# Kernel optimization log

Hardware: AMD Instinct MI355X
Metric: run time of the kernel (lower is better)

The kernel has to match this reference:

```python
import jax, jax.numpy as jnp
import numpy as np

C = 1024
H = 16
HS = C // H
HID = 4096
A_MIX = 0.7
B_MIX = 0.3
EPS = 1e-5


def layernorm(x, w, b):
    mu = jnp.mean(x, axis=-1, keepdims=True)
    var = jnp.mean(jnp.square(x - mu), axis=-1, keepdims=True)
    return (x - mu) * jax.lax.rsqrt(var + EPS) * w + b


def setup_inputs() -> dict:
    key = jax.random.key(0)
    ks = jax.random.split(key, 12)
    B, N = 4, 1024
    s = 1.0 / np.sqrt(C)
    sh = 1.0 / np.sqrt(HID)
    return {
        "x": jax.random.normal(ks[0], (B, N, C), jnp.float32),
        "Query": jax.random.normal(ks[1], (B, H, N, HS), jnp.float32),
        "Key": jax.random.normal(ks[2], (B, H, N, HS), jnp.float32),
        "Value": jax.random.normal(ks[3], (B, H, N, HS), jnp.float32),
        "ln_w": jnp.ones((C,), jnp.float32),
        "ln_b": jnp.zeros((C,), jnp.float32),
        "qk_w": jax.random.normal(ks[4], (2 * C, C), jnp.float32) * s,
        "qk_b": jnp.zeros((2 * C,), jnp.float32),
        "v_w": jax.random.normal(ks[5], (C, C), jnp.float32) * s,
        "v_b": jnp.zeros((C,), jnp.float32),
        "out_w": jax.random.normal(ks[6], (C, C), jnp.float32) * s,
        "out_b": jnp.zeros((C,), jnp.float32),
        "mlp_w1": jax.random.normal(ks[7], (HID, C), jnp.float32) * s,
        "mlp_b1": jnp.zeros((HID,), jnp.float32),
        "mlp_w2": jax.random.normal(ks[8], (C, HID), jnp.float32) * sh,
        "mlp_b2": jnp.zeros((C,), jnp.float32),
    }


def reference(x, Query, Key, Value, ln_w, ln_b, qk_w, qk_b, v_w, v_b,
              out_w, out_b, mlp_w1, mlp_b1, mlp_w2, mlp_b2):
    B, N, _ = x.shape
    x1 = x
    xn = layernorm(x, ln_w, ln_b)
    # qk projection -> view (B,N,H,HS,2), permute -> (2,B,H,N,HS)
    qk = (xn @ qk_w.T + qk_b).reshape(B, N, H, HS, 2)
    Q = jnp.transpose(qk[..., 0], (0, 2, 1, 3))  # (B,H,N,HS)
    K = jnp.transpose(qk[..., 1], (0, 2, 1, 3))
    V = jnp.transpose((xn @ v_w.T + v_b).reshape(B, N, H, HS), (0, 2, 1, 3))
    Query = A_MIX * Q + B_MIX * Query
    Key = A_MIX * K + B_MIX * Key
    Value = B_MIX * Value + A_MIX * V
    attn = jnp.einsum('bhqd,bhkd->bhqk', Query, Key) / np.sqrt(HS)
    attn = jax.nn.softmax(attn, axis=-1)  # dropout = identity in eval
    o = jnp.einsum('bhqk,bhkd->bhqd', attn, Value)
    o = jnp.transpose(o, (0, 2, 1, 3)).reshape(B, N, C)
    o = o @ out_w.T + out_b
    x = x1 + o
    x2 = x
    xn2 = layernorm(x, ln_w, ln_b)  # same layernorm params reused
    h = jax.nn.gelu(xn2 @ mlp_w1.T + mlp_b1, approximate=False)
    m = h @ mlp_w2.T + mlp_b2
    return (m + x2, Query, Key, Value)
```

## Files before the change

kernel.cpp:

```cpp
#include <hip/hip_runtime.h>

using bf16x8 = __attribute__((ext_vector_type(8))) __bf16;
using f32x4  = __attribute__((ext_vector_type(4))) float;

#define AS1(p) (const __attribute__((address_space(1))) void*)(p)
#define AS3(p) (__attribute__((address_space(3))) void*)(p)

__device__ __forceinline__ unsigned short f2bf(float f) {
    unsigned int u = __float_as_uint(f);
    unsigned int r = (u + 0x7FFFu + ((u >> 16) & 1u)) >> 16;
    return (unsigned short)r;
}
__device__ __forceinline__ float bf2f(unsigned short u) {
    return __uint_as_float((unsigned int)u << 16);
}

__global__ __launch_bounds__(256) void cvt_kernel(const float* __restrict__ in,
                                                  unsigned short* __restrict__ out,
                                                  int n) {
    int i = (blockIdx.x * 256 + threadIdx.x) * 4;
    if (i < n) {
        float4 v = *(const float4*)(in + i);
        ushort4 o = make_ushort4(f2bf(v.x), f2bf(v.y), f2bf(v.z), f2bf(v.w));
        *(ushort4*)(out + i) = o;
    }
}

__global__ __launch_bounds__(256) void ln_kernel(const float* __restrict__ in,
                                                 const float* __restrict__ w,
                                                 const float* __restrict__ b,
                                                 unsigned short* __restrict__ out) {
    const int row = blockIdx.x;
    const int tid = threadIdx.x;
    const float4 v = *(const float4*)(in + (size_t)row * 1024 + tid * 4);
    float s  = v.x + v.y + v.z + v.w;
    float ss = v.x * v.x + v.y * v.y + v.z * v.z + v.w * v.w;
    #pragma unroll
    for (int m = 1; m < 64; m <<= 1) {
        s  += __shfl_xor(s, m, 64);
        ss += __shfl_xor(ss, m, 64);
    }
    __shared__ float red[8];
    if ((tid & 63) == 0) { red[(tid >> 6) * 2] = s; red[(tid >> 6) * 2 + 1] = ss; }
    __syncthreads();
    s  = red[0] + red[2] + red[4] + red[6];
    ss = red[1] + red[3] + red[5] + red[7];
    const float mu  = s * (1.0f / 1024.0f);
    const float var = ss * (1.0f / 1024.0f) - mu * mu;
    const float rstd = rsqrtf(var + 1e-5f);
    const float4 wv = *(const float4*)(w + tid * 4);
    const float4 bv = *(const float4*)(b + tid * 4);
    ushort4 o;
    o.x = f2bf((v.x - mu) * rstd * wv.x + bv.x);
    o.y = f2bf((v.y - mu) * rstd * wv.y + bv.y);
    o.z = f2bf((v.z - mu) * rstd * wv.z + bv.z);
    o.w = f2bf((v.w - mu) * rstd * wv.w + bv.w);
    *(ushort4*)(out + (size_t)row * 1024 + tid * 4) = o;
}

template <int EPI>
__global__ __launch_bounds__(256, 4)
void gemm_bt(const unsigned short* __restrict__ A,
             const unsigned short* __restrict__ W,
             const float* __restrict__ bias,
             int M, int N, int K,
             const float* __restrict__ e0, const float* __restrict__ e1,
             float* __restrict__ o0, float* __restrict__ o1,
             unsigned short* __restrict__ u0, unsigned short* __restrict__ u1) {
    __shared__ unsigned short As0[128 * 32];
    __shared__ unsigned short Bs0[128 * 32];
    __shared__ unsigned short As1[128 * 32];
    __shared__ unsigned short Bs1[128 * 32];
    const int tid  = threadIdx.x;
    const int wave = tid >> 6, lane = tid & 63;
    const int wr = wave >> 1, wc = wave & 1;
    const int q15 = lane & 15, g = lane >> 4;
    const int gm0 = blockIdx.y * 128, gn0 = blockIdx.x * 128;

    f32x4 acc[4][4] = {};

    const int srow16 = lane >> 2;
    const int sslot  = (((lane & 3) ^ (srow16 & 3) ^ ((srow16 >> 2) & 3)) << 3);
    const int rx     = ((q15 ^ (q15 >> 2)) & 3) << 4;

    const unsigned short* Arow = A + (size_t)(gm0 + wave * 32 + srow16) * K + sslot;
    const unsigned short* Wrow = W + (size_t)(gn0 + wave * 32 + srow16) * K + sslot;
    const size_t rstep = (size_t)16 * K;

    #define STAGE(kt, Asb, Bsb)                                                         \
        {                                                                               \
            const int k0_ = (kt) * 32;                                                  \
            __builtin_amdgcn_global_load_lds(AS1(Arow + k0_),                           \
                AS3((char*)Asb + wave * 2048), 16, 0, 0);                               \
            __builtin_amdgcn_global_load_lds(AS1(Arow + rstep + k0_),                   \
                AS3((char*)Asb + wave * 2048 + 1024), 16, 0, 0);                        \
            __builtin_amdgcn_global_load_lds(AS1(Wrow + k0_),                           \
                AS3((char*)Bsb + wave * 2048), 16, 0, 0);                               \
            __builtin_amdgcn_global_load_lds(AS1(Wrow + rstep + k0_),                   \
                AS3((char*)Bsb + wave * 2048 + 1024), 16, 0, 0);                        \
        }

    #define COMPUTE(Asb, Bsb)                                                           \
        {                                                                               \
            bf16x8 af[4], bfr[4];                                                       \
            _Pragma("unroll")                                                           \
            for (int m = 0; m < 4; ++m)                                                 \
                af[m] = *(const bf16x8*)((char*)Asb +                                   \
                         (wr * 64 + m * 16 + q15) * 64 + ((g << 4) ^ rx));              \
            _Pragma("unroll")                                                           \
            for (int n = 0; n < 4; ++n)                                                 \
                bfr[n] = *(const bf16x8*)((char*)Bsb +                                  \
                         (wc * 64 + n * 16 + q15) * 64 + ((g << 4) ^ rx));              \
            _Pragma("unroll")                                                           \
            for (int m = 0; m < 4; ++m)                                                 \
                _Pragma("unroll")                                                       \
                for (int n = 0; n < 4; ++n)                                             \
                    acc[m][n] = __builtin_amdgcn_mfma_f32_16x16x32_bf16(                \
                        af[m], bfr[n], acc[m][n], 0, 0, 0);                             \
        }

    const int nt = K >> 5;
    STAGE(0, As0, Bs0);
    __syncthreads();
    for (int t = 0; t + 2 < nt; t += 2) {
        STAGE(t + 1, As1, Bs1);
        COMPUTE(As0, Bs0);
        __syncthreads();
        STAGE(t + 2, As0, Bs0);
        COMPUTE(As1, Bs1);
        __syncthreads();
    }
    STAGE(nt - 1, As1, Bs1);
    COMPUTE(As0, Bs0);
    __syncthreads();
    COMPUTE(As1, Bs1);
    #undef STAGE
    #undef COMPUTE

    #pragma unroll
    for (int m = 0; m < 4; ++m)
    #pragma unroll
    for (int n = 0; n < 4; ++n)
    #pragma unroll
    for (int j = 0; j < 4; ++j) {
        const int r = gm0 + wr * 64 + m * 16 + g * 4 + j;
        const int c = gn0 + wc * 64 + n * 16 + q15;
        const float val = acc[m][n][j] + bias[c];
        if constexpr (EPI == 0) {
            const int bb = r >> 10, nn = r & 1023;
            const int h = c >> 7, hs = (c >> 1) & 63, isk = c & 1;
            const size_t idx = (((size_t)(bb * 16 + h)) * 1024 + nn) * 64 + hs;
            if (!isk) { const float mx = 0.7f * val + 0.3f * e0[idx]; o0[idx] = mx; u0[idx] = f2bf(mx); }
            else      { const float mx = 0.7f * val + 0.3f * e1[idx]; o1[idx] = mx; u1[idx] = f2bf(mx); }
        } else if constexpr (EPI == 1) {
            const int bb = r >> 10, nn = r & 1023;
            const int h = c >> 6, hs = c & 63;
            const size_t idx = (((size_t)(bb * 16 + h)) * 1024 + nn) * 64 + hs;
            const float mx = 0.7f * val + 0.3f * e0[idx];
            o0[idx] = mx;
            u0[(((size_t)(bb * 16 + h)) * 64 + hs) * 1024 + nn] = f2bf(mx);
        } else if constexpr (EPI == 2) {
            const size_t idx = (size_t)r * N + c;
            o0[idx] = val + e0[idx];
        } else if constexpr (EPI == 3) {
            const float gg = 0.5f * val * (1.0f + erff(val * 0.70710678118f));
            u0[(size_t)r * N + c] = f2bf(gg);
        } else {
            const size_t idx = (size_t)r * N + c;
            o0[idx] = val + e0[idx];
        }
    }
}

__global__ __launch_bounds__(256, 6)
void attn_kernel(const unsigned short* __restrict__ Qb,
                 const unsigned short* __restrict__ Kb,
                 const unsigned short* __restrict__ Vt,
                 unsigned short* __restrict__ Op,
                 float* __restrict__ Mws,
                 float* __restrict__ Lws) {
    const int bh = blockIdx.y;
    const int z  = blockIdx.z;
    const int tid = threadIdx.x, wave = tid >> 6, lane = tid & 63;
    const int qbase = blockIdx.x * 64 + wave * 16;
    const int q15 = lane & 15, g = lane >> 4;

    const unsigned short* Qh = Qb + (size_t)bh * 1024 * 64;
    const unsigned short* Kh = Kb + (size_t)bh * 1024 * 64;
    const unsigned short* Vh = Vt + (size_t)bh * 64 * 1024;

    __shared__ alignas(128) unsigned short Ks[64 * 64];
    __shared__ alignas(128) unsigned short Vs[64 * 64];
    __shared__ alignas(128) unsigned short Ps[4][1024];
    char* const Pb = (char*)Ps[wave] + q15 * 128;
    const int swz = (q15 & 7) << 4;

    const int srow8 = lane >> 3;
    const int selm  = (((lane & 7) ^ srow8) << 3);

    bf16x8 aq[2];
    aq[0] = *(const bf16x8*)&Qh[(size_t)(qbase + q15) * 64 + 0  + g * 8];
    aq[1] = *(const bf16x8*)&Qh[(size_t)(qbase + q15) * 64 + 32 + g * 8];

    f32x4 o[4] = {};
    float mrow = -1e30f, lrow = 0.f;

    const int t0 = z * 8;
    for (int t = t0; t < t0 + 8; ++t) {
        const int kb = t * 64;
        #pragma unroll
        for (int i = 0; i < 2; ++i) {
            const int r = wave * 16 + i * 8 + srow8;
            __builtin_amdgcn_global_load_lds(AS1(Kh + (size_t)(kb + r) * 64 + selm),
                                             AS3((char*)Ks + wave * 2048 + i * 1024), 16, 0, 0);
            __builtin_amdgcn_global_load_lds(AS1(Vh + (size_t)r * 1024 + kb + selm),
                                             AS3((char*)Vs + wave * 2048 + i * 1024), 16, 0, 0);
        }
        __syncthreads();

        f32x4 s[4] = {};
        #pragma unroll
        for (int kt = 0; kt < 4; ++kt) {
            #pragma unroll
            for (int kk = 0; kk < 2; ++kk) {
                const bf16x8 bk = *(const bf16x8*)((char*)Ks + (kt * 16 + q15) * 128 +
                                                   ((kk * 64 + g * 16) ^ swz));
                s[kt] = __builtin_amdgcn_mfma_f32_16x16x32_bf16(bk, aq[kk], s[kt], 0, 0, 0);
            }
        }
        float pm = -1e30f;
        #pragma unroll
        for (int kt = 0; kt < 4; ++kt) {
            s[kt] *= 0.125f;
            pm = fmaxf(pm, fmaxf(fmaxf(s[kt][0], s[kt][1]), fmaxf(s[kt][2], s[kt][3])));
        }
        pm = fmaxf(pm, __shfl_xor(pm, 16, 64));
        pm = fmaxf(pm, __shfl_xor(pm, 32, 64));
        const float mnew = fmaxf(mrow, pm);
        const float alpha = __expf(mrow - mnew);
        mrow = mnew;

        float rs = 0.f;
        #pragma unroll
        for (int kt = 0; kt < 4; ++kt) {
            const float p0 = __expf(s[kt][0] - mnew);
            const float p1 = __expf(s[kt][1] - mnew);
            const float p2 = __expf(s[kt][2] - mnew);
            const float p3 = __expf(s[kt][3] - mnew);
            rs += (p0 + p1) + (p2 + p3);
            uint2 pk;
            pk.x = (unsigned int)f2bf(p0) | ((unsigned int)f2bf(p1) << 16);
            pk.y = (unsigned int)f2bf(p2) | ((unsigned int)f2bf(p3) << 16);
            *(uint2*)(Pb + (((kt * 32 + g * 8) ^ swz))) = pk;
        }
        rs += __shfl_xor(rs, 16, 64);
        rs += __shfl_xor(rs, 32, 64);
        lrow = lrow * alpha + rs;

        float af[4];
        #pragma unroll
        for (int j = 0; j < 4; ++j) af[j] = __shfl(alpha, g * 4 + j, 64);
        #pragma unroll
        for (int dt = 0; dt < 4; ++dt)
            #pragma unroll
            for (int j = 0; j < 4; ++j) o[dt][j] *= af[j];

        #pragma unroll
        for (int Bb = 0; Bb < 2; ++Bb) {
            const bf16x8 pa = *(const bf16x8*)(Pb + (((Bb * 64 + g * 16) ^ swz)));
            #pragma unroll
            for (int dt = 0; dt < 4; ++dt) {
                const bf16x8 vb = *(const bf16x8*)((char*)Vs + (dt * 16 + q15) * 128 +
                                                   ((Bb * 64 + g * 16) ^ swz));
                o[dt] = __builtin_amdgcn_mfma_f32_16x16x32_bf16(pa, vb, o[dt], 0, 0, 0);
            }
        }
        __syncthreads();
    }

    #pragma unroll
    for (int dt = 0; dt < 4; ++dt)
        #pragma unroll
        for (int j = 0; j < 4; ++j) {
            const int q = qbase + g * 4 + j;
            Op[(((size_t)z * 64 + bh) * 1024 + q) * 64 + dt * 16 + q15] = f2bf(o[dt][j]);
        }
    if (g == 0) {
        const size_t mi = ((size_t)z * 64 + bh) * 1024 + qbase + q15;
        Mws[mi] = mrow;
        Lws[mi] = lrow;
    }
}

__global__ __launch_bounds__(256)
void attn_combine(const unsigned short* __restrict__ Op,
                  const float* __restrict__ Mws,
                  const float* __restrict__ Lws,
                  unsigned short* __restrict__ Ob) {
    const int e4 = blockIdx.x * 256 + threadIdx.x;
    const int d0 = (e4 & 15) * 4;
    const int q  = (e4 >> 4) & 1023;
    const int bh = e4 >> 14;
    const size_t base0 = (((size_t)bh) * 1024 + q) * 64 + d0;
    const size_t base1 = (((size_t)(64 + bh)) * 1024 + q) * 64 + d0;
    const ushort4 a = *(const ushort4*)&Op[base0];
    const ushort4 c = *(const ushort4*)&Op[base1];
    const size_t mi0 = (size_t)bh * 1024 + q;
    const size_t mi1 = mi0 + 64 * 1024;
    const float m0 = Mws[mi0], m1 = Mws[mi1];
    const float l0 = Lws[mi0], l1 = Lws[mi1];
    const float m  = fmaxf(m0, m1);
    const float w0 = __expf(m0 - m), w1 = __expf(m1 - m);
    const float inv = 1.0f / (l0 * w0 + l1 * w1);
    ushort4 r;
    r.x = f2bf((bf2f(a.x) * w0 + bf2f(c.x) * w1) * inv);
    r.y = f2bf((bf2f(a.y) * w0 + bf2f(c.y) * w1) * inv);
    r.z = f2bf((bf2f(a.z) * w0 + bf2f(c.z) * w1) * inv);
    r.w = f2bf((bf2f(a.w) * w0 + bf2f(c.w) * w1) * inv);
    const int b = bh >> 4, h = bh & 15;
    *(ushort4*)&Ob[((size_t)(b * 1024 + q)) * 1024 + h * 64 + d0] = r;
}

extern "C" void kernel_launch(void* const* d_in, const int* in_sizes, int n_in,
                              void* d_out, int out_size, void* d_ws, size_t ws_size,
                              hipStream_t stream) {
    (void)in_sizes; (void)n_in; (void)out_size; (void)ws_size;
    const float* x     = (const float*)d_in[0];
    const float* Qin   = (const float*)d_in[1];
    const float* Kin   = (const float*)d_in[2];
    const float* Vin   = (const float*)d_in[3];
    const float* ln_w  = (const float*)d_in[4];
    const float* ln_b  = (const float*)d_in[5];
    const float* qk_w  = (const float*)d_in[6];
    const float* qk_b  = (const float*)d_in[7];
    const float* v_w   = (const float*)d_in[8];
    const float* v_b   = (const float*)d_in[9];
    const float* out_w = (const float*)d_in[10];
    const float* out_b = (const float*)d_in[11];
    const float* w1    = (const float*)d_in[12];
    const float* b1    = (const float*)d_in[13];
    const float* w2    = (const float*)d_in[14];
    const float* b2    = (const float*)d_in[15];

    const size_t FOUR_M = (size_t)4 * 1024 * 1024;
    float* out0 = (float*)d_out;
    float* Qout = out0 + FOUR_M;
    float* Kout = Qout + FOUR_M;
    float* Vout = Kout + FOUR_M;

    char* ws = (char*)d_ws;
    const size_t MB = 1024 * 1024;
    unsigned short* xn   = (unsigned short*)(ws + 0);
    unsigned short* qkwb = (unsigned short*)(ws + 8 * MB);
    unsigned short* vwb  = (unsigned short*)(ws + 12 * MB);
    unsigned short* owb  = (unsigned short*)(ws + 14 * MB);
    unsigned short* w1b  = (unsigned short*)(ws + 16 * MB);
    unsigned short* w2b  = (unsigned short*)(ws + 24 * MB);
    unsigned short* Qbuf = (unsigned short*)(ws + 32 * MB);
    unsigned short* Kbuf = (unsigned short*)(ws + 40 * MB);
    unsigned short* Vtb  = (unsigned short*)(ws + 48 * MB);
    unsigned short* atto = (unsigned short*)(ws + 56 * MB);
    unsigned short* hbuf = (unsigned short*)(ws + 32 * MB);
    float* y1 = (float*)(ws + 64 * MB);
    unsigned short* Oprt = (unsigned short*)(ws + 64 * MB);
    float* Mws = (float*)(ws + 8 * MB);
    float* Lws = (float*)(ws + 8 * MB + 512 * 1024);

    cvt_kernel<<<2048, 256, 0, stream>>>(qk_w, qkwb, 2048 * 1024);
    cvt_kernel<<<1024, 256, 0, stream>>>(v_w,  vwb,  1024 * 1024);
    cvt_kernel<<<1024, 256, 0, stream>>>(out_w, owb, 1024 * 1024);
    cvt_kernel<<<4096, 256, 0, stream>>>(w1, w1b, 4096 * 1024);
    cvt_kernel<<<4096, 256, 0, stream>>>(w2, w2b, 4096 * 1024);

    ln_kernel<<<4096, 256, 0, stream>>>(x, ln_w, ln_b, xn);

    {
        dim3 g(2048 / 128, 4096 / 128);
        gemm_bt<0><<<g, 256, 0, stream>>>(xn, qkwb, qk_b, 4096, 2048, 1024,
                                          Qin, Kin, Qout, Kout, Qbuf, Kbuf);
    }
    {
        dim3 g(1024 / 128, 4096 / 128);
        gemm_bt<1><<<g, 256, 0, stream>>>(xn, vwb, v_b, 4096, 1024, 1024,
                                          Vin, nullptr, Vout, nullptr, Vtb, nullptr);
    }
    {
        dim3 g(16, 64, 2);
        attn_kernel<<<g, 256, 0, stream>>>(Qbuf, Kbuf, Vtb, Oprt, Mws, Lws);
        attn_combine<<<4096, 256, 0, stream>>>(Oprt, Mws, Lws, atto);
    }
    {
        dim3 g(1024 / 128, 4096 / 128);
        gemm_bt<2><<<g, 256, 0, stream>>>(atto, owb, out_b, 4096, 1024, 1024,
                                          x, nullptr, y1, nullptr, nullptr, nullptr);
    }
    ln_kernel<<<4096, 256, 0, stream>>>(y1, ln_w, ln_b, xn);
    {
        dim3 g(4096 / 128, 4096 / 128);
        gemm_bt<3><<<g, 256, 0, stream>>>(xn, w1b, b1, 4096, 4096, 1024,
                                          nullptr, nullptr, nullptr, nullptr, hbuf, nullptr);
    }
    {
        dim3 g(1024 / 128, 4096 / 128);
        gemm_bt<4><<<g, 256, 0, stream>>>(hbuf, w2b, b2, 4096, 1024, 4096,
                                          y1, nullptr, out0, nullptr, nullptr, nullptr);
    }
}
```

Measured before the change: 308.6 us.

## Deepen GEMM LDS pipeline to four stages with explicit vmcnt waits

Replaces the double-buffered LDS staging in the bf16 GEMM with a four-deep ring buffer. Explicit s_waitcnt vmcnt counts and raw s_barrier calls replace __syncthreads, so up to three tiles of global-to-LDS loads stay in flight while one is computed. The LDS swizzle pattern is also changed, and launch bounds drop from 4 to 2 blocks per SM to fit the doubled shared memory. This trades occupancy for deeper latency hiding. The hand-written waitcnt logic assumes exactly four loads per stage and that the compiler emits no other vector memory ops in the loop.

```diff
diff --git a/kernel.cpp b/kernel.cpp
--- a/kernel.cpp
+++ b/kernel.cpp
@@ -59,7 +59,7 @@
 }
 
 template <int EPI>
-__global__ __launch_bounds__(256, 4)
+__global__ __launch_bounds__(256, 2)
 void gemm_bt(const unsigned short* __restrict__ A,
              const unsigned short* __restrict__ W,
              const float* __restrict__ bias,
@@ -67,10 +67,8 @@
              const float* __restrict__ e0, const float* __restrict__ e1,
              float* __restrict__ o0, float* __restrict__ o1,
              unsigned short* __restrict__ u0, unsigned short* __restrict__ u1) {
-    __shared__ unsigned short As0[128 * 32];
-    __shared__ unsigned short Bs0[128 * 32];
-    __shared__ unsigned short As1[128 * 32];
-    __shared__ unsigned short Bs1[128 * 32];
+    __shared__ unsigned short As[4][128 * 32];
+    __shared__ unsigned short Bs[4][128 * 32];
     const int tid  = threadIdx.x;
     const int wave = tid >> 6, lane = tid & 63;
     const int wr = wave >> 1, wc = wave & 1;
@@ -79,37 +77,36 @@
 
     f32x4 acc[4][4] = {};
 
-    const int srow16 = lane >> 2;
-    const int sslot  = (((lane & 3) ^ (srow16 & 3) ^ ((srow16 >> 2) & 3)) << 3);
-    const int rx     = ((q15 ^ (q15 >> 2)) & 3) << 4;
-
-    const unsigned short* Arow = A + (size_t)(gm0 + wave * 32 + srow16) * K + sslot;
-    const unsigned short* Wrow = W + (size_t)(gn0 + wave * 32 + srow16) * K + sslot;
+    const int selm = (((lane & 3) ^ ((lane >> 3) & 3)) << 3);
+    const int rx   = ((q15 >> 1) & 3) << 4;
+
+    const unsigned short* Arow = A + (size_t)(gm0 + wave * 32 + (lane >> 2)) * K + selm;
+    const unsigned short* Wrow = W + (size_t)(gn0 + wave * 32 + (lane >> 2)) * K + selm;
     const size_t rstep = (size_t)16 * K;
 
-    #define STAGE(kt, Asb, Bsb)                                                         \
+    #define STAGE(kt, b)                                                                \
         {                                                                               \
             const int k0_ = (kt) * 32;                                                  \
             __builtin_amdgcn_global_load_lds(AS1(Arow + k0_),                           \
-                AS3((char*)Asb + wave * 2048), 16, 0, 0);                               \
+                AS3((char*)As[b] + wave * 2048), 16, 0, 0);                             \
             __builtin_amdgcn_global_load_lds(AS1(Arow + rstep + k0_),                   \
-                AS3((char*)Asb + wave * 2048 + 1024), 16, 0, 0);                        \
+                AS3((char*)As[b] + wave * 2048 + 1024), 16, 0, 0);                      \
             __builtin_amdgcn_global_load_lds(AS1(Wrow + k0_),                           \
-                AS3((char*)Bsb + wave * 2048), 16, 0, 0);                               \
+                AS3((char*)Bs[b] + wave * 2048), 16, 0, 0);                             \
             __builtin_amdgcn_global_load_lds(AS1(Wrow + rstep + k0_),                   \
-                AS3((char*)Bsb + wave * 2048 + 1024), 16, 0, 0);                        \
-        }
-
-    #define COMPUTE(Asb, Bsb)                                                           \
+                AS3((char*)Bs[b] + wave * 2048 + 1024), 16, 0, 0);                      \
+        }
+
+    #define COMPUTE(b)                                                                  \
         {                                                                               \
             bf16x8 af[4], bfr[4];                                                       \
             _Pragma("unroll")                                                           \
             for (int m = 0; m < 4; ++m)                                                 \
-                af[m] = *(const bf16x8*)((char*)Asb +                                   \
+                af[m] = *(const bf16x8*)((char*)As[b] +                                 \
                          (wr * 64 + m * 16 + q15) * 64 + ((g << 4) ^ rx));              \
             _Pragma("unroll")                                                           \
             for (int n = 0; n < 4; ++n)                                                 \
-                bfr[n] = *(const bf16x8*)((char*)Bsb +                                  \
+                bfr[n] = *(const bf16x8*)((char*)Bs[b] +                                \
                          (wc * 64 + n * 16 + q15) * 64 + ((g << 4) ^ rx));              \
             _Pragma("unroll")                                                           \
             for (int m = 0; m < 4; ++m)                                                 \
@@ -120,20 +117,22 @@
         }
 
     const int nt = K >> 5;
-    STAGE(0, As0, Bs0);
-    __syncthreads();
-    for (int t = 0; t + 2 < nt; t += 2) {
-        STAGE(t + 1, As1, Bs1);
-        COMPUTE(As0, Bs0);
-        __syncthreads();
-        STAGE(t + 2, As0, Bs0);
-        COMPUTE(As1, Bs1);
-        __syncthreads();
-    }
-    STAGE(nt - 1, As1, Bs1);
-    COMPUTE(As0, Bs0);
-    __syncthreads();
-    COMPUTE(As1, Bs1);
+    STAGE(0, 0); STAGE(1, 1); STAGE(2, 2); STAGE(3, 3);
+    int cur = 0;
+    for (int t = 0; t < nt; ++t) {
+        const int rem = nt - 1 - t;
+        if (rem >= 3)      asm volatile("s_waitcnt vmcnt(12)" ::: "memory");
+        else if (rem == 2) asm volatile("s_waitcnt vmcnt(8)"  ::: "memory");
+        else if (rem == 1) asm volatile("s_waitcnt vmcnt(4)"  ::: "memory");
+        else               asm volatile("s_waitcnt vmcnt(0)"  ::: "memory");
+        __builtin_amdgcn_s_barrier();
+        COMPUTE(cur);
+        if (t + 4 < nt) {
+            __builtin_amdgcn_s_barrier();
+            STAGE(t + 4, cur);
+        }
+        cur = (cur + 1) & 3;
+    }
     #undef STAGE
     #undef COMPUTE
 
```

Result: slower. 318.8 us (+3.3%).
